# Optimization experiments

Measured on AMD Instinct MI355X. Metric: run time of the kernel, lower is better.

The kernel has to match this reference:

```python
import jax, jax.numpy as jnp
import numpy as np

BETA = 0.25  # commitment_cost


def setup_inputs() -> dict:
    key = jax.random.key(0)
    k1, k2 = jax.random.split(key)
    N, K, D = 32768, 8192, 512
    z = jax.random.normal(k1, (N, D), dtype=jnp.float32)
    # mimic nn.init.uniform_(codebook, -1/K, 1/K)
    codebook = jax.random.uniform(k2, (K, D), dtype=jnp.float32,
                                  minval=-1.0 / K, maxval=1.0 / K)
    return {"z": z, "codebook": codebook}


def reference(z, codebook):
    # squared L2 distances: ||z||^2 + ||c||^2 - 2 z c^T   -> [N, K]
    d = (jnp.sum(z * z, axis=1, keepdims=True)
         + jnp.sum(codebook * codebook, axis=1)
         - 2.0 * (z @ codebook.T))
    indices = jnp.argmin(d, axis=1)            # [N] int
    z_q = codebook[indices]                    # [N, D] gather (grad flows to codebook)
    # commit_loss = beta * mse(z.detach(), z_q)
    commit_loss = BETA * jnp.mean((jax.lax.stop_gradient(z) - z_q) ** 2)
    # straight-through estimator
    z_st = z + jax.lax.stop_gradient(z_q - z)
    return z_st, indices, commit_loss
```

## Files before the change

kernel.cpp:

```cpp
#include <hip/hip_runtime.h>
#include <cfloat>
#include <cstdint>
#include <cstddef>

#define N_ROWS 32768
#define K_CODES 8192
#define DIM 512
#define BETA 0.25

typedef unsigned short u16;
typedef _Float16 half8 __attribute__((ext_vector_type(8)));
typedef float f32x4 __attribute__((ext_vector_type(4)));

#define BM 256
#define BN 256
#define SKH 32
#define NPH (DIM / SKH)
#define OVCAP 512
#define DELTA_A 0.4f

#define GLOAD_LDS16(g, l)                                          \
  __builtin_amdgcn_global_load_lds(                                \
      (const __attribute__((address_space(1))) void*)(g),          \
      (__attribute__((address_space(3))) void*)(l), 16, 0, 0)

__device__ inline u16 f2h(float x) {
  union { _Float16 h; u16 u; } c;
  c.h = (_Float16)x;
  return c.u;
}

__global__ __launch_bounds__(256)
void vq_cvt(const float* __restrict__ src, u16* __restrict__ dst, float scale,
            int n8, int* ovcnt_reset) {
  if (ovcnt_reset != nullptr && blockIdx.x == 0 && threadIdx.x == 0) *ovcnt_reset = 0;
  int i = blockIdx.x * 256 + threadIdx.x;
  if (i >= n8) return;
  float4 a = ((const float4*)src)[(size_t)i * 2];
  float4 b = ((const float4*)src)[(size_t)i * 2 + 1];
  uint4 o;
  o.x = (unsigned)f2h(a.x * scale) | ((unsigned)f2h(a.y * scale) << 16);
  o.y = (unsigned)f2h(a.z * scale) | ((unsigned)f2h(a.w * scale) << 16);
  o.z = (unsigned)f2h(b.x * scale) | ((unsigned)f2h(b.y * scale) << 16);
  o.w = (unsigned)f2h(b.z * scale) | ((unsigned)f2h(b.w * scale) << 16);
  ((uint4*)dst)[i] = o;
}

__global__ __launch_bounds__(256)
void vq_s1(const float* __restrict__ z, float* __restrict__ s1out) {
  int row = blockIdx.x * 256 + threadIdx.x;
  const float* p = z + (size_t)row * DIM;
  float lf[4];
#pragma unroll
  for (int L = 0; L < 4; ++L) {
    const float* q = p + L * 128;
    float r[8];
#pragma unroll
    for (int j = 0; j < 8; ++j) r[j] = __fmul_rn(q[j], q[j]);
    for (int i = 8; i < 128; i += 8) {
#pragma unroll
      for (int j = 0; j < 8; ++j)
        r[j] = __fadd_rn(r[j], __fmul_rn(q[i + j], q[i + j]));
    }
    float s01 = __fadd_rn(r[0], r[1]);
    float s23 = __fadd_rn(r[2], r[3]);
    float s45 = __fadd_rn(r[4], r[5]);
    float s67 = __fadd_rn(r[6], r[7]);
    lf[L] = __fadd_rn(__fadd_rn(s01, s23), __fadd_rn(s45, s67));
  }
  s1out[row] = __fadd_rn(__fadd_rn(lf[0], lf[1]), __fadd_rn(lf[2], lf[3]));
}

__global__ __launch_bounds__(512, 2)
void vq_gemm(const u16* __restrict__ zh, const u16* __restrict__ ch,
             float* __restrict__ tilemax, uint2* __restrict__ ovlist,
             int* __restrict__ ovcnt, int gcap) {
  __shared__ u16 ring[4][16384];
  __shared__ float rmaxw[4][BM];
  __shared__ uint2 obuf[OVCAP];
  __shared__ int ocnt, gbase;
  const int tid = threadIdx.x;
  const int lane = tid & 63;
  const int wid = tid >> 6;
  const int wrow = (wid >> 2) * 128;
  const int wcol = (wid & 3) * 64;
  const int wg = blockIdx.x;
  const int xcd = wg & 7;
  const int kk = wg >> 3;
  const int colb = xcd * 4 + (kk & 3);
  const int rowb = kk >> 2;
  const int col0 = colb * BN;
  const int row0 = rowb * BM;
  if (tid == 0) ocnt = 0;

  f32x4 acc[8][4];
#pragma unroll
  for (int m = 0; m < 8; ++m)
#pragma unroll
    for (int n = 0; n < 4; ++n) acc[m][n] = (f32x4){0.f, 0.f, 0.f, 0.f};

  const int arow = tid >> 2;
  const int sslot8 = (((tid & 3) ^ ((tid >> 3) & 3))) * 8;
  const u16* pa0 = zh + (size_t)(row0 + arow) * DIM + sslot8;
  const u16* pa1 = pa0 + (size_t)128 * DIM;
  const u16* pb0 = ch + (size_t)(col0 + arow) * DIM + sslot8;
  const u16* pb1 = pb0 + (size_t)128 * DIM;
  const unsigned dof = tid * 8;

#define STAGE(s)                                              \
  {                                                           \
    u16* sl_ = ring[(s) & 3];                                 \
    GLOAD_LDS16(pa0 + (s) * SKH, sl_ + dof);                  \
    GLOAD_LDS16(pa1 + (s) * SKH, sl_ + 4096 + dof);           \
    GLOAD_LDS16(pb0 + (s) * SKH, sl_ + 8192 + dof);           \
    GLOAD_LDS16(pb1 + (s) * SKH, sl_ + 12288 + dof);          \
  }

  const int xorv = ((lane >> 4) ^ ((lane >> 1) & 3)) << 4;
  const int aoff = (wrow + (lane & 15)) * 64 + xorv;
  const int boff = 16384 + (wcol + (lane & 15)) * 64 + xorv;

  STAGE(0);
  STAGE(1);

#pragma unroll
  for (int s = 0; s < NPH; ++s) {
    if (s + 2 < NPH) STAGE(s + 2);
    if (s < NPH - 2) {
      asm volatile("s_waitcnt vmcnt(8)" ::: "memory");
    } else if (s == NPH - 2) {
      asm volatile("s_waitcnt vmcnt(4)" ::: "memory");
    } else {
      asm volatile("s_waitcnt vmcnt(0)" ::: "memory");
    }
    __builtin_amdgcn_sched_barrier(0);
    __builtin_amdgcn_s_barrier();
    const char* sl = (const char*)ring[s & 3];
    half8 af[8], bf[4];
#pragma unroll
    for (int m = 0; m < 8; ++m)
      af[m] = *(const half8*)(sl + aoff + m * 1024);
#pragma unroll
    for (int n = 0; n < 4; ++n)
      bf[n] = *(const half8*)(sl + boff + n * 1024);
    asm volatile("s_waitcnt lgkmcnt(0)" ::: "memory");
    __builtin_amdgcn_sched_barrier(0);
    __builtin_amdgcn_s_setprio(1);
#pragma unroll
    for (int m = 0; m < 8; ++m)
#pragma unroll
      for (int n = 0; n < 4; ++n)
        acc[m][n] = __builtin_amdgcn_mfma_f32_16x16x32_f16(af[m], bf[n],
                                                           acc[m][n], 0, 0, 0);
    __builtin_amdgcn_s_setprio(0);
  }
#undef STAGE

  const int wn = wid & 3;
#pragma unroll
  for (int m = 0; m < 8; ++m) {
#pragma unroll
    for (int rg = 0; rg < 4; ++rg) {
      float mx = acc[m][0][rg];
#pragma unroll
      for (int n = 1; n < 4; ++n) mx = fmaxf(mx, acc[m][n][rg]);
#pragma unroll
      for (int s = 1; s <= 8; s <<= 1) mx = fmaxf(mx, __shfl_xor(mx, s, 64));
      int Rloc = wrow + m * 16 + (lane >> 4) * 4 + rg;
      if ((lane & 15) == 0) rmaxw[wn][Rloc] = mx;
    }
  }
  __syncthreads();
#pragma unroll
  for (int m = 0; m < 8; ++m) {
#pragma unroll
    for (int rg = 0; rg < 4; ++rg) {
      int Rloc = wrow + m * 16 + (lane >> 4) * 4 + rg;
      int grow = row0 + Rloc;
      float gm = fmaxf(fmaxf(rmaxw[0][Rloc], rmaxw[1][Rloc]),
                       fmaxf(rmaxw[2][Rloc], rmaxw[3][Rloc]));
      if (wn == 0 && (lane & 15) == 0)
        tilemax[(size_t)colb * N_ROWS + grow] = gm;
      float thr = gm - DELTA_A;
#pragma unroll
      for (int n = 0; n < 4; ++n) {
        float v = acc[m][n][rg];
        if (v >= thr) {
          int code = col0 + wcol + n * 16 + (lane & 15);
          uint2 e = make_uint2(((unsigned)grow << 13) | (unsigned)code,
                               __float_as_uint(v));
          int p = atomicAdd(&ocnt, 1);
          if (p < OVCAP) obuf[p] = e;
          else {
            int g = atomicAdd(ovcnt, 1);
            if (g < gcap) ovlist[g] = e;
          }
        }
      }
    }
  }
  __syncthreads();
  int n = ocnt < OVCAP ? ocnt : OVCAP;
  if (tid == 0) gbase = atomicAdd(ovcnt, n);
  __syncthreads();
  for (int i = tid; i < n; i += 512) {
    int g = gbase + i;
    if (g < gcap) ovlist[g] = obuf[i];
  }
}

__global__ __launch_bounds__(256)
void vq_merge(const float* __restrict__ tilemax, float* __restrict__ mthr,
              unsigned long long* __restrict__ win) {
  int row = blockIdx.x * 256 + threadIdx.x;
  float g = -1e30f;
  for (int t = 0; t < K_CODES / BN; ++t)
    g = fmaxf(g, tilemax[(size_t)t * N_ROWS + row]);
  mthr[row] = g - DELTA_A;
  win[row] = ~0ULL;
}

__global__ __launch_bounds__(256)
void vq_init(unsigned long long* __restrict__ win) {
  int row = blockIdx.x * 256 + threadIdx.x;
  win[row] = ~0ULL;
}

__global__ __launch_bounds__(256)
void vq_overflow(const float* __restrict__ z, const float* __restrict__ cb,
                 const float* __restrict__ s1, const float* __restrict__ mthr,
                 const uint2* __restrict__ ovlist, const int* __restrict__ ovcnt,
                 int gcap, unsigned long long* __restrict__ win) {
  int n = *ovcnt;
  if (n > gcap) n = gcap;
  for (int i = blockIdx.x * 256 + threadIdx.x; i < n; i += gridDim.x * 256) {
    uint2 e = ovlist[i];
    int row = e.x >> 13;
    int code = e.x & 8191;
    if (__uint_as_float(e.y) < mthr[row]) continue;
    const float* zp = z + (size_t)row * DIM;
    const float* cp = cb + (size_t)code * DIM;
    float acc = 0.f;
    for (int k = 0; k < DIM; k += 4) {
      float4 zv = *(const float4*)(zp + k);
      float4 cv = *(const float4*)(cp + k);
      acc = fmaf(zv.x, cv.x, acc);
      acc = fmaf(zv.y, cv.y, acc);
      acc = fmaf(zv.z, cv.z, acc);
      acc = fmaf(zv.w, cv.w, acc);
    }
    float dq = __fsub_rn(s1[row], __fmul_rn(2.0f, acc));
    unsigned long long key =
        ((unsigned long long)__float_as_uint(dq) << 32) | (unsigned)code;
    atomicMin(&win[row], key);
  }
}

__global__ __launch_bounds__(256)
void vq_fallback(const float* __restrict__ z, const float* __restrict__ cb,
                 const float* __restrict__ s1, const int* __restrict__ ovcnt,
                 int gcap, int force, unsigned long long* __restrict__ win) {
  if (!force && *ovcnt <= gcap) return;
  __shared__ float zrow[DIM];
  __shared__ unsigned long long red[256];
  for (int row = blockIdx.x; row < N_ROWS; row += gridDim.x) {
    __syncthreads();
    for (int t = threadIdx.x; t < DIM; t += 256) zrow[t] = z[(size_t)row * DIM + t];
    __syncthreads();
    float s1v = s1[row];
    unsigned long long best = ~0ULL;
    for (int j = threadIdx.x; j < K_CODES; j += 256) {
      const float* cp = cb + (size_t)j * DIM;
      float acc = 0.f;
      for (int k = 0; k < DIM; ++k) acc = fmaf(zrow[k], cp[k], acc);
      float dq = __fsub_rn(s1v, __fmul_rn(2.0f, acc));
      unsigned long long key =
          ((unsigned long long)__float_as_uint(dq) << 32) | (unsigned)j;
      if (key < best) best = key;
    }
    red[threadIdx.x] = best;
    __syncthreads();
    for (int s = 128; s > 0; s >>= 1) {
      if (threadIdx.x < s && red[threadIdx.x + s] < red[threadIdx.x])
        red[threadIdx.x] = red[threadIdx.x + s];
      __syncthreads();
    }
    if (threadIdx.x == 0) atomicMin(&win[row], red[0]);
    __syncthreads();
  }
}

__global__ __launch_bounds__(256)
void vq_out(const float* __restrict__ z, const float* __restrict__ cb,
            const unsigned long long* __restrict__ win, float* __restrict__ out,
            double* __restrict__ loss64) {
  int wid = threadIdx.x >> 6, lane = threadIdx.x & 63;
  int row = blockIdx.x * 4 + wid;
  int I1 = (int)(win[row] & 8191ULL);
  const float* zp = z + (size_t)row * DIM + lane * 8;
  const float* cp = cb + (size_t)I1 * DIM + lane * 8;
  float4 z0 = *(const float4*)zp, z1 = *(const float4*)(zp + 4);
  float4 c0 = *(const float4*)cp, c1 = *(const float4*)(cp + 4);
  *(float4*)&out[(size_t)row * DIM + lane * 8] = c0;
  *(float4*)&out[(size_t)row * DIM + lane * 8 + 4] = c1;
  double s = 0.0, d;
  d = (double)z0.x - c0.x; s += d * d;
  d = (double)z0.y - c0.y; s += d * d;
  d = (double)z0.z - c0.z; s += d * d;
  d = (double)z0.w - c0.w; s += d * d;
  d = (double)z1.x - c1.x; s += d * d;
  d = (double)z1.y - c1.y; s += d * d;
  d = (double)z1.z - c1.z; s += d * d;
  d = (double)z1.w - c1.w; s += d * d;
#pragma unroll
  for (int m = 32; m >= 1; m >>= 1) s += __shfl_down(s, m, 64);
  if (lane == 0) {
    loss64[row] = s;
    out[(size_t)N_ROWS * DIM + row] = (float)I1;
  }
}

__global__ __launch_bounds__(1024)
void vq_loss(const double* __restrict__ loss64, float* __restrict__ out) {
  __shared__ double sd[1024];
  double s = 0.0;
  for (int i = threadIdx.x; i < N_ROWS; i += 1024) s += loss64[i];
  sd[threadIdx.x] = s;
  __syncthreads();
  for (int k = 512; k > 0; k >>= 1) {
    if (threadIdx.x < k) sd[threadIdx.x] += sd[threadIdx.x + k];
    __syncthreads();
  }
  if (threadIdx.x == 0)
    out[(size_t)N_ROWS * DIM + N_ROWS] =
        (float)(BETA * sd[0] / ((double)N_ROWS * (double)DIM));
}

extern "C" void kernel_launch(void* const* d_in, const int* in_sizes, int n_in,
                              void* d_out, int out_size, void* d_ws, size_t ws_size,
                              hipStream_t stream) {
  const float* z = (const float*)d_in[0];
  const float* cb = (const float*)d_in[1];
  float* out = (float*)d_out;
  char* ws = (char*)d_ws;

  const size_t OFF_ZH = 0;
  const size_t OFF_CH = 33554432;
  const size_t OFF_S1 = 41943040;
  const size_t OFF_MT = 42074112;
  const size_t OFF_WIN = 42205184;
  const size_t OFF_L64 = 42467328;
  const size_t OFF_TM = 42729472;
  const size_t OFF_OC = 51118080;
  const size_t OFF_OV = 51118096;
  const size_t MIN_FAST = OFF_OV + (size_t)8 * 1024 * 1024;

  if (ws_size >= MIN_FAST) {
    u16* zh = (u16*)(ws + OFF_ZH);
    u16* ch = (u16*)(ws + OFF_CH);
    float* s1f = (float*)(ws + OFF_S1);
    float* mthr = (float*)(ws + OFF_MT);
    unsigned long long* win = (unsigned long long*)(ws + OFF_WIN);
    double* loss64 = (double*)(ws + OFF_L64);
    float* tilemax = (float*)(ws + OFF_TM);
    int* ovcnt = (int*)(ws + OFF_OC);
    uint2* ovlist = (uint2*)(ws + OFF_OV);
    long long gc = (long long)(ws_size - OFF_OV) / 8;
    if (gc > 6 * 1024 * 1024) gc = 6 * 1024 * 1024;
    int gcap = (int)gc;

    vq_cvt<<<N_ROWS * DIM / 8 / 256, 256, 0, stream>>>(z, zh, 1.0f,
                                                       N_ROWS * DIM / 8, ovcnt);
    vq_cvt<<<K_CODES * DIM / 8 / 256, 256, 0, stream>>>(cb, ch, 4096.0f,
                                                        K_CODES * DIM / 8, nullptr);
    vq_s1<<<N_ROWS / 256, 256, 0, stream>>>(z, s1f);
    vq_gemm<<<dim3((K_CODES / BN) * (N_ROWS / BM)), 512, 0, stream>>>(
        zh, ch, tilemax, ovlist, ovcnt, gcap);
    vq_merge<<<N_ROWS / 256, 256, 0, stream>>>(tilemax, mthr, win);
    vq_overflow<<<2048, 256, 0, stream>>>(z, cb, s1f, mthr, ovlist, ovcnt, gcap, win);
    vq_fallback<<<2048, 256, 0, stream>>>(z, cb, s1f, ovcnt, gcap, 0, win);
    vq_out<<<N_ROWS / 4, 256, 0, stream>>>(z, cb, win, out, loss64);
    vq_loss<<<1, 1024, 0, stream>>>(loss64, out);
  } else {
    float* s1f = (float*)(ws + 0);
    unsigned long long* win = (unsigned long long*)(ws + 131072);
    double* loss64 = (double*)(ws + 393216);
    vq_s1<<<N_ROWS / 256, 256, 0, stream>>>(z, s1f);
    vq_init<<<N_ROWS / 256, 256, 0, stream>>>(win);
    vq_fallback<<<2048, 256, 0, stream>>>(z, cb, s1f, nullptr, 0, 1, win);
    vq_out<<<N_ROWS / 4, 256, 0, stream>>>(z, cb, win, out, loss64);
    vq_loss<<<1, 1024, 0, stream>>>(loss64, out);
  }
}
```

Before: 669.9 us.

## Restructure GEMM mainloop to double-buffered 64-wide K tiles with split prefetch

Replaces the 4-slot ring of 32-wide K stages with two 64-wide K buffers for A and B, using a new 8-way XOR swizzle. Each K tile is processed in four quarter-steps (two M halves times two K sub-steps), and the next tile's global-to-LDS loads are spread over the first two quarters. The aim is fewer stage synchronisations and better interleaving of loads with MFMA work. In exchange it adds two barriers per quarter and a full vmcnt(0) drain at the end of each tile, leaving only one tile of prefetch depth.

```diff
diff --git a/kernel.cpp b/kernel.cpp
--- a/kernel.cpp
+++ b/kernel.cpp
@@ -14,8 +14,8 @@
 
 #define BM 256
 #define BN 256
-#define SKH 32
-#define NPH (DIM / SKH)
+#define BKH 64
+#define NT (DIM / BKH)
 #define OVCAP 512
 #define DELTA_A 0.4f
 
@@ -75,7 +75,8 @@
 void vq_gemm(const u16* __restrict__ zh, const u16* __restrict__ ch,
              float* __restrict__ tilemax, uint2* __restrict__ ovlist,
              int* __restrict__ ovcnt, int gcap) {
-  __shared__ u16 ring[4][16384];
+  __shared__ u16 Ah[2][BM * BKH];
+  __shared__ u16 Bh[2][BN * BKH];
   __shared__ float rmaxw[4][BM];
   __shared__ uint2 obuf[OVCAP];
   __shared__ int ocnt, gbase;
@@ -99,62 +100,77 @@
 #pragma unroll
     for (int n = 0; n < 4; ++n) acc[m][n] = (f32x4){0.f, 0.f, 0.f, 0.f};
 
-  const int arow = tid >> 2;
-  const int sslot8 = (((tid & 3) ^ ((tid >> 3) & 3))) * 8;
-  const u16* pa0 = zh + (size_t)(row0 + arow) * DIM + sslot8;
-  const u16* pa1 = pa0 + (size_t)128 * DIM;
-  const u16* pb0 = ch + (size_t)(col0 + arow) * DIM + sslot8;
-  const u16* pb1 = pb0 + (size_t)128 * DIM;
-  const unsigned dof = tid * 8;
-
-#define STAGE(s)                                              \
-  {                                                           \
-    u16* sl_ = ring[(s) & 3];                                 \
-    GLOAD_LDS16(pa0 + (s) * SKH, sl_ + dof);                  \
-    GLOAD_LDS16(pa1 + (s) * SKH, sl_ + 4096 + dof);           \
-    GLOAD_LDS16(pb0 + (s) * SKH, sl_ + 8192 + dof);           \
-    GLOAD_LDS16(pb1 + (s) * SKH, sl_ + 12288 + dof);          \
-  }
-
-  const int xorv = ((lane >> 4) ^ ((lane >> 1) & 3)) << 4;
-  const int aoff = (wrow + (lane & 15)) * 64 + xorv;
-  const int boff = 16384 + (wcol + (lane & 15)) * 64 + xorv;
-
-  STAGE(0);
-  STAGE(1);
-
-#pragma unroll
-  for (int s = 0; s < NPH; ++s) {
-    if (s + 2 < NPH) STAGE(s + 2);
-    if (s < NPH - 2) {
-      asm volatile("s_waitcnt vmcnt(8)" ::: "memory");
-    } else if (s == NPH - 2) {
-      asm volatile("s_waitcnt vmcnt(4)" ::: "memory");
-    } else {
+  const int sslot8 = ((tid & 7) ^ ((tid >> 3) & 7)) * 8;
+  const u16* pa[4];
+  const u16* pb[4];
+  unsigned lofs[4];
+#pragma unroll
+  for (int c = 0; c < 4; ++c) {
+    pa[c] = zh + (size_t)(row0 + c * 64 + (tid >> 3)) * DIM + sslot8;
+    pb[c] = ch + (size_t)(col0 + c * 64 + (tid >> 3)) * DIM + sslot8;
+    lofs[c] = c * 4096 + tid * 8;
+  }
+
+  const int oA0 = (wrow + (lane & 15)) * 128;
+  const int oB0 = (wcol + (lane & 15)) * 128;
+  int colk[2];
+#pragma unroll
+  for (int ks = 0; ks < 2; ++ks)
+    colk[ks] = (((lane >> 4) + 4 * ks) ^ (lane & 7)) << 4;
+
+#pragma unroll
+  for (int c = 0; c < 4; ++c) {
+    GLOAD_LDS16(pa[c], (u16*)Ah[0] + lofs[c]);
+    GLOAD_LDS16(pb[c], (u16*)Bh[0] + lofs[c]);
+  }
+  asm volatile("s_waitcnt vmcnt(0)" ::: "memory");
+  __builtin_amdgcn_s_barrier();
+
+  half8 bf[4];
+#pragma unroll
+  for (int t = 0; t < NT; ++t) {
+    const int cur = t & 1;
+    const char* A = (const char*)Ah[cur];
+    const char* B = (const char*)Bh[cur];
+#pragma unroll
+    for (int q = 0; q < 4; ++q) {
+      const int mh = q & 1;
+      const int ks = q >> 1;
+      if (t + 1 < NT && q < 2) {
+        u16* An = (u16*)Ah[cur ^ 1];
+        u16* Bn = (u16*)Bh[cur ^ 1];
+        const int c0 = q * 2, c1 = q * 2 + 1;
+        GLOAD_LDS16(pa[c0] + (t + 1) * BKH, An + lofs[c0]);
+        GLOAD_LDS16(pa[c1] + (t + 1) * BKH, An + lofs[c1]);
+        GLOAD_LDS16(pb[c0] + (t + 1) * BKH, Bn + lofs[c0]);
+        GLOAD_LDS16(pb[c1] + (t + 1) * BKH, Bn + lofs[c1]);
+      }
+      half8 af[4];
+      if (mh == 0) {
+#pragma unroll
+        for (int n = 0; n < 4; ++n)
+          bf[n] = *(const half8*)(B + oB0 + n * 2048 + colk[ks]);
+      }
+#pragma unroll
+      for (int m = 0; m < 4; ++m)
+        af[m] = *(const half8*)(A + oA0 + mh * 8192 + m * 2048 + colk[ks]);
+      __builtin_amdgcn_s_barrier();
+      asm volatile("s_waitcnt lgkmcnt(0)" ::: "memory");
+      __builtin_amdgcn_sched_barrier(0);
+      __builtin_amdgcn_s_setprio(1);
+#pragma unroll
+      for (int m = 0; m < 4; ++m)
+#pragma unroll
+        for (int n = 0; n < 4; ++n)
+          acc[mh * 4 + m][n] = __builtin_amdgcn_mfma_f32_16x16x32_f16(
+              af[m], bf[n], acc[mh * 4 + m][n], 0, 0, 0);
+      __builtin_amdgcn_s_setprio(0);
+      __builtin_amdgcn_s_barrier();
+    }
+    if (t + 1 < NT) {
       asm volatile("s_waitcnt vmcnt(0)" ::: "memory");
     }
-    __builtin_amdgcn_sched_barrier(0);
-    __builtin_amdgcn_s_barrier();
-    const char* sl = (const char*)ring[s & 3];
-    half8 af[8], bf[4];
-#pragma unroll
-    for (int m = 0; m < 8; ++m)
-      af[m] = *(const half8*)(sl + aoff + m * 1024);
-#pragma unroll
-    for (int n = 0; n < 4; ++n)
-      bf[n] = *(const half8*)(sl + boff + n * 1024);
-    asm volatile("s_waitcnt lgkmcnt(0)" ::: "memory");
-    __builtin_amdgcn_sched_barrier(0);
-    __builtin_amdgcn_s_setprio(1);
-#pragma unroll
-    for (int m = 0; m < 8; ++m)
-#pragma unroll
-      for (int n = 0; n < 4; ++n)
-        acc[m][n] = __builtin_amdgcn_mfma_f32_16x16x32_f16(af[m], bf[n],
-                                                           acc[m][n], 0, 0, 0);
-    __builtin_amdgcn_s_setprio(0);
-  }
-#undef STAGE
+  }
 
   const int wn = wid & 3;
 #pragma unroll
```

After: 720.3 us. +7.5%, slower.
